# Performance work log

Hardware: AMD Instinct MI355X
Metric: run time of the kernel (lower is better)

The kernel has to match this reference:

```python
import jax, jax.numpy as jnp
import numpy as np

E, B, D, H, Z = 8, 16384, 512, 512, 64   # experts, batch, input_dim, hidden, latent
NHID = 2                                 # num_mlp_layers - 1 hidden-to-hidden layers


def setup_inputs() -> dict:
    key = jax.random.key(0)
    ks = jax.random.split(key, 12)

    def w(k, shape, fan_in):
        return (jax.random.normal(k, shape, jnp.float32) / np.sqrt(fan_in)).astype(jnp.float32)

    return {
        "x": jax.random.normal(ks[0], (B, D), jnp.float32),
        "eps": jax.random.normal(ks[1], (B, Z), jnp.float32),
        # stacked per-expert parameters (leading axis E)
        "enc_in_w": w(ks[2], (E, D, H), D), "enc_in_b": jnp.zeros((E, H), jnp.float32),
        "enc_hid_w": w(ks[3], (E, NHID, H, H), H), "enc_hid_b": jnp.zeros((E, NHID, H), jnp.float32),
        "mu_w": w(ks[4], (E, H, Z), H), "mu_b": jnp.zeros((E, Z), jnp.float32),
        "lv_w": w(ks[5], (E, H, Z), H), "lv_b": jnp.zeros((E, Z), jnp.float32),
        "dec_in_w": w(ks[6], (E, Z, H), Z), "dec_in_b": jnp.zeros((E, H), jnp.float32),
        "dec_hid_w": w(ks[7], (E, NHID, H, H), H), "dec_hid_b": jnp.zeros((E, NHID, H), jnp.float32),
        "dec_out_w": w(ks[8], (E, H, D), H), "dec_out_b": jnp.zeros((E, D), jnp.float32),
    }


def _moe_forward(x, eps, enc_in_w, enc_in_b, enc_hid_w, enc_hid_b,
                 mu_w, mu_b, lv_w, lv_b,
                 dec_in_w, dec_in_b, dec_hid_w, dec_hid_b, dec_out_w, dec_out_b):
    # ---- every expert tries the problem (dense, all experts over full batch) ----
    h = jax.nn.relu(jnp.einsum('bd,edh->ebh', x, enc_in_w) + enc_in_b[:, None, :])
    for i in range(NHID):
        h = jax.nn.relu(jnp.einsum('ebh,ehk->ebk', h, enc_hid_w[:, i]) + enc_hid_b[:, i, None, :])
    mu = jnp.einsum('ebh,ehz->ebz', h, mu_w) + mu_b[:, None, :]          # [E,B,Z]
    logvar = jnp.einsum('ebh,ehz->ebz', h, lv_w) + lv_b[:, None, :]       # [E,B,Z]
    z = mu + jnp.exp(0.5 * logvar) * eps[None, :, :]                      # reparameterize
    g = jax.nn.relu(jnp.einsum('ebz,ezh->ebh', z, dec_in_w) + dec_in_b[:, None, :])
    for i in range(NHID):
        g = jax.nn.relu(jnp.einsum('ebh,ehk->ebk', g, dec_hid_w[:, i]) + dec_hid_b[:, i, None, :])
    xhat = jnp.einsum('ebh,ehd->ebd', g, dec_out_w) + dec_out_b[:, None, :]  # [E,B,D]

    # ---- per-sample recon loss, pick best expert (torch.min over experts) ----
    recon = jnp.mean((xhat - x[None, :, :]) ** 2, axis=-1)                # [E,B]
    expert_idx = jnp.argmin(recon, axis=0)                                # [B]

    # ---- sparse_others: single fused gather instead of python loop ----
    bi = jnp.arange(x.shape[0])
    return mu[expert_idx, bi], logvar[expert_idx, bi], xhat[expert_idx, bi]


def reference(x, eps, enc_in_w, enc_in_b, enc_hid_w, enc_hid_b,
              mu_w, mu_b, lv_w, lv_b,
              dec_in_w, dec_in_b, dec_hid_w, dec_hid_b, dec_out_w, dec_out_b):
    return _moe_forward(x, eps, enc_in_w, enc_in_b, enc_hid_w, enc_hid_b,
                        mu_w, mu_b, lv_w, lv_b,
                        dec_in_w, dec_in_b, dec_hid_w, dec_hid_b, dec_out_w, dec_out_b)
```

## Files before the change

kernel.cpp:

```cpp
#include <hip/hip_runtime.h>
#include <cstdint>

#define Eexp 8
#define Bb   16384
#define Dd   512
#define Hh   512
#define Zz   64

typedef _Float16 f16x8 __attribute__((ext_vector_type(8)));
typedef float    f32x4 __attribute__((ext_vector_type(4)));

#define OFF_ENCIN  0
#define OFF_HID0   524288
#define OFF_HID1   1048576
#define OFF_HEADS  1572864
#define OFF_DECIN  1703936
#define OFF_DHID0  1769472
#define OFF_DHID1  2293760
#define OFF_DECOUT 2818048
#define PEREXP     3342336
#define WT_TOTAL   (8 * (size_t)PEREXP)

#define GLL16(g, l) __builtin_amdgcn_global_load_lds( \
    (const __attribute__((address_space(1))) void*)(g), \
    (__attribute__((address_space(3))) void*)(l), 16, 0, 0)

template<bool TR>
__global__ __launch_bounds__(256)
void fmsplit(const float* __restrict__ src, _Float16* __restrict__ dst,
             int KTOT, int inner, long sStride, long dStride)
{
    __shared__ float t[64][65];
    const int e  = blockIdx.z;
    const int o0 = blockIdx.x * 64;
    const int k0 = blockIdx.y * 64;
    const float* S = src + (size_t)e * sStride;
    _Float16*    D = dst + (size_t)e * dStride;
    const int tid = threadIdx.x;
    const int rr = tid >> 4, c4 = (tid & 15) * 4;
    #pragma unroll
    for (int p = 0; p < 4; ++p) {
        const int r = rr + p * 16;
        const float4 v = *reinterpret_cast<const float4*>(
            S + (size_t)(TR ? (k0 + r) : (o0 + r)) * inner + (TR ? o0 : k0) + c4);
        t[r][c4 + 0] = v.x; t[r][c4 + 1] = v.y;
        t[r][c4 + 2] = v.z; t[r][c4 + 3] = v.w;
    }
    __syncthreads();
    const int lane = tid & 63, wid = tid >> 6;
    const int KB = KTOT >> 5;
    #pragma unroll
    for (int p = 0; p < 2; ++p) {
        const int g  = wid * 2 + p;
        const int ot = g >> 1, kb = g & 1;
        const int rI = ot * 16 + (lane & 15);
        const int kI = kb * 32 + (lane >> 4) * 8;
        f16x8 hv, lv;
        #pragma unroll
        for (int j = 0; j < 8; ++j) {
            const float v = TR ? t[kI + j][rI] : t[rI][kI + j];
            const _Float16 h = (_Float16)v;
            hv[j] = h; lv[j] = (_Float16)(v - (float)h);
        }
        const size_t base = ((size_t)((o0 >> 4) + ot) * KB + (k0 >> 5) + kb) * 1024;
        *reinterpret_cast<f16x8*>(D + base + lane * 8)       = hv;
        *reinterpret_cast<f16x8*>(D + base + 512 + lane * 8) = lv;
    }
}

template<int KA>
__global__ __launch_bounds__(256, 2)
void gemm_mid(const _Float16* __restrict__ Afm, const _Float16* __restrict__ Wfm,
              const float* __restrict__ bias0, _Float16* __restrict__ Cfm)
{
    constexpr int KB  = KA / 32;
    constexpr int NT  = KB;
    constexpr int ACH = 16;
    constexpr int NCH = 32;
    constexpr int GPW = 8;
    __shared__ __align__(16) _Float16 lds[2 * NCH * 512];

    const int bid = blockIdx.x;
    const int bx = (bid & 7) * 16 + (bid >> 5);
    const int by = (bid >> 3) & 3;

    const int lane = threadIdx.x & 63, wid = threadIdx.x >> 6;
    const int wr = wid >> 1, wc = wid & 1;
    const int row0 = bx * 128;
    const int col0 = by * 128;

    const _Float16* src[GPW];
    #pragma unroll
    for (int p = 0; p < GPW; ++p) {
        const int q = wid * GPW + p;
        if (q < ACH)
            src[p] = Afm + (size_t)((row0 >> 4) + (q >> 1)) * KB * 1024
                         + (q & 1) * 512 + lane * 8;
        else {
            const int qq = q - ACH;
            src[p] = Wfm + (size_t)((col0 >> 4) + (qq >> 1)) * KB * 1024
                         + (qq & 1) * 512 + lane * 8;
        }
    }

    f32x4 acc[4][4];
    #pragma unroll
    for (int i = 0; i < 4; ++i)
        #pragma unroll
        for (int j = 0; j < 4; ++j) acc[i][j] = {0.f, 0.f, 0.f, 0.f};

#define STAGE(buf)                                                           \
    { _Pragma("unroll")                                                      \
      for (int p = 0; p < GPW; ++p) {                                        \
          GLL16(src[p], lds + (buf) * (NCH * 512) + (wid * GPW + p) * 512);  \
          src[p] += 1024;                                                    \
      } }

    STAGE(0)
    if (NT > 1) STAGE(1)

    for (int t = 0; t < NT; ++t) {
        if (t + 1 < NT) { asm volatile("s_waitcnt vmcnt(%0)" :: "i"(GPW) : "memory"); }
        else            { asm volatile("s_waitcnt vmcnt(0)" ::: "memory"); }
        __builtin_amdgcn_s_barrier();
        asm volatile("" ::: "memory");

        const _Float16* B0 = lds + (t & 1) * (NCH * 512);
        f16x8 ah[4], al[4], wh[4], wl[4];
        #pragma unroll
        for (int mf = 0; mf < 4; ++mf) {
            const int q = (wr * 4 + mf) * 2;
            ah[mf] = *reinterpret_cast<const f16x8*>(B0 + q * 512 + lane * 8);
            al[mf] = *reinterpret_cast<const f16x8*>(B0 + q * 512 + 512 + lane * 8);
        }
        #pragma unroll
        for (int nf = 0; nf < 4; ++nf) {
            const int q = ACH + (wc * 4 + nf) * 2;
            wh[nf] = *reinterpret_cast<const f16x8*>(B0 + q * 512 + lane * 8);
            wl[nf] = *reinterpret_cast<const f16x8*>(B0 + q * 512 + 512 + lane * 8);
        }
        __builtin_amdgcn_s_setprio(1);
        #pragma unroll
        for (int mf = 0; mf < 4; ++mf)
            #pragma unroll
            for (int nf = 0; nf < 4; ++nf) {
                acc[mf][nf] = __builtin_amdgcn_mfma_f32_16x16x32_f16(
                    ah[mf], wh[nf], acc[mf][nf], 0, 0, 0);
                acc[mf][nf] = __builtin_amdgcn_mfma_f32_16x16x32_f16(
                    ah[mf], wl[nf], acc[mf][nf], 0, 0, 0);
                acc[mf][nf] = __builtin_amdgcn_mfma_f32_16x16x32_f16(
                    al[mf], wh[nf], acc[mf][nf], 0, 0, 0);
            }
        __builtin_amdgcn_s_setprio(0);
        asm volatile("" ::: "memory");
        __builtin_amdgcn_s_barrier();
        asm volatile("" ::: "memory");
        if (t + 2 < NT) STAGE(t & 1)
    }
#undef STAGE

    uint32_t* sb = reinterpret_cast<uint32_t*>(&lds[0]);
    #pragma unroll
    for (int ph = 0; ph < 2; ++ph) {
        if (wc == ph) {
            #pragma unroll
            for (int nf = 0; nf < 4; ++nf) {
                const int c_l = nf * 16 + (lane & 15);
                const float bv = bias0[col0 + ph * 64 + c_l];
                #pragma unroll
                for (int mf = 0; mf < 4; ++mf)
                    #pragma unroll
                    for (int j = 0; j < 4; ++j) {
                        const int r_l = wr * 64 + mf * 16 + (lane >> 4) * 4 + j;
                        const float v = fmaxf(acc[mf][nf][j] + bv, 0.f);
                        const _Float16 h = (_Float16)v;
                        const _Float16 lo = (_Float16)(v - (float)h);
                        const uint32_t pk =
                            (uint32_t)__builtin_bit_cast(uint16_t, h) |
                            ((uint32_t)__builtin_bit_cast(uint16_t, lo) << 16);
                        sb[r_l * 64 + (((c_l >> 2) ^ (r_l & 15)) << 2) + (c_l & 3)] = pk;
                    }
            }
        }
        __syncthreads();
        {
            #pragma unroll
            for (int i = 0; i < 4; ++i) {
                const int q = wid * 4 + i;
                const int T_l = q >> 1, kb_l = q & 1;
                const int r_l = T_l * 16 + (lane & 15);
                const int cb  = kb_l * 32 + (lane >> 4) * 8;
                uint32_t u[8];
                #pragma unroll
                for (int jb = 0; jb < 2; ++jb) {
                    const int chunk = ((cb >> 2) + jb) ^ (r_l & 15);
                    const uint32_t* pp = &sb[r_l * 64 + chunk * 4];
                    u[jb*4+0] = pp[0]; u[jb*4+1] = pp[1];
                    u[jb*4+2] = pp[2]; u[jb*4+3] = pp[3];
                }
                f16x8 hv, lvv;
                #pragma unroll
                for (int j = 0; j < 8; ++j) {
                    hv[j]  = __builtin_bit_cast(_Float16, (uint16_t)(u[j] & 0xffff));
                    lvv[j] = __builtin_bit_cast(_Float16, (uint16_t)(u[j] >> 16));
                }
                const size_t base =
                    ((size_t)((row0 >> 4) + T_l) * 16 +
                     ((col0 + ph * 64) >> 5) + kb_l) * 1024;
                *reinterpret_cast<f16x8*>(Cfm + base + lane * 8)       = hv;
                *reinterpret_cast<f16x8*>(Cfm + base + 512 + lane * 8) = lvv;
            }
        }
        __syncthreads();
    }
}

__global__ __launch_bounds__(256, 2)
void heads_z(const _Float16* __restrict__ Afm, const _Float16* __restrict__ Wfm,
             const float* __restrict__ mu_b, const float* __restrict__ lv_b,
             const float* __restrict__ eps,
             float* __restrict__ mu_e, float* __restrict__ lv_e,
             _Float16* __restrict__ zfm)
{
    constexpr int KB = 16, NT = 16, ACH = 8, NCH = 24, GPW = 6;
    __shared__ __align__(16) _Float16 lds[2 * NCH * 512];

    const int bid = blockIdx.x;
    const int bx = (bid & 7) * 32 + (bid >> 3);
    const int lane = threadIdx.x & 63, wid = threadIdx.x >> 6;
    const int wr = wid >> 1, wc = wid & 1;
    const int row0 = bx * 64;

    const _Float16* src[GPW];
    #pragma unroll
    for (int p = 0; p < GPW; ++p) {
        const int q = wid * GPW + p;
        if (q < ACH)
            src[p] = Afm + (size_t)((row0 >> 4) + (q >> 1)) * KB * 1024
                         + (q & 1) * 512 + lane * 8;
        else {
            const int qq = q - ACH;
            src[p] = Wfm + (size_t)(qq >> 1) * KB * 1024 + (qq & 1) * 512 + lane * 8;
        }
    }

    f32x4 acc[2][4];
    #pragma unroll
    for (int i = 0; i < 2; ++i)
        #pragma unroll
        for (int j = 0; j < 4; ++j) acc[i][j] = {0.f, 0.f, 0.f, 0.f};

#define STAGE(buf)                                                           \
    { _Pragma("unroll")                                                      \
      for (int p = 0; p < GPW; ++p) {                                        \
          GLL16(src[p], lds + (buf) * (NCH * 512) + (wid * GPW + p) * 512);  \
          src[p] += 1024;                                                    \
      } }

    STAGE(0)
    STAGE(1)

    for (int t = 0; t < NT; ++t) {
        if (t + 1 < NT) { asm volatile("s_waitcnt vmcnt(%0)" :: "i"(GPW) : "memory"); }
        else            { asm volatile("s_waitcnt vmcnt(0)" ::: "memory"); }
        __builtin_amdgcn_s_barrier();
        asm volatile("" ::: "memory");

        const _Float16* B0 = lds + (t & 1) * (NCH * 512);
        f16x8 ah[2], al[2], wh[4], wl[4];
        #pragma unroll
        for (int mf = 0; mf < 2; ++mf) {
            const int q = (wr * 2 + mf) * 2;
            ah[mf] = *reinterpret_cast<const f16x8*>(B0 + q * 512 + lane * 8);
            al[mf] = *reinterpret_cast<const f16x8*>(B0 + q * 512 + 512 + lane * 8);
        }
        #pragma unroll
        for (int nf = 0; nf < 4; ++nf) {
            const int q = ACH + (wc * 4 + nf) * 2;
            wh[nf] = *reinterpret_cast<const f16x8*>(B0 + q * 512 + lane * 8);
            wl[nf] = *reinterpret_cast<const f16x8*>(B0 + q * 512 + 512 + lane * 8);
        }
        __builtin_amdgcn_s_setprio(1);
        #pragma unroll
        for (int mf = 0; mf < 2; ++mf)
            #pragma unroll
            for (int nf = 0; nf < 4; ++nf) {
                acc[mf][nf] = __builtin_amdgcn_mfma_f32_16x16x32_f16(
                    ah[mf], wh[nf], acc[mf][nf], 0, 0, 0);
                acc[mf][nf] = __builtin_amdgcn_mfma_f32_16x16x32_f16(
                    ah[mf], wl[nf], acc[mf][nf], 0, 0, 0);
                acc[mf][nf] = __builtin_amdgcn_mfma_f32_16x16x32_f16(
                    al[mf], wh[nf], acc[mf][nf], 0, 0, 0);
            }
        __builtin_amdgcn_s_setprio(0);
        asm volatile("" ::: "memory");
        __builtin_amdgcn_s_barrier();
        asm volatile("" ::: "memory");
        if (t + 2 < NT) STAGE(t & 1)
    }
#undef STAGE

    float* mulv = reinterpret_cast<float*>(&lds[0]);
    #pragma unroll
    for (int nf = 0; nf < 4; ++nf) {
        const int c_h = wc * 64 + nf * 16 + (lane & 15);
        const float bv = (c_h < 64) ? mu_b[c_h] : lv_b[c_h - 64];
        #pragma unroll
        for (int mf = 0; mf < 2; ++mf)
            #pragma unroll
            for (int j = 0; j < 4; ++j) {
                const int r_l = wr * 32 + mf * 16 + (lane >> 4) * 4 + j;
                mulv[r_l * 128 + c_h] = acc[mf][nf][j] + bv;
            }
    }
    __syncthreads();
    const int tid = threadIdx.x;
    #pragma unroll
    for (int k = 0; k < 16; ++k) {
        const int id  = tid + k * 256;
        const int r_l = id >> 6, c = id & 63;
        const float m = mulv[r_l * 128 + c];
        const float l = mulv[r_l * 128 + 64 + c];
        const size_t go = (size_t)(row0 + r_l) * 64 + c;
        const float ev = eps[go];
        const float z  = m + expf(0.5f * l) * ev;
        mu_e[go] = m; lv_e[go] = l;
        const _Float16 h  = (_Float16)z;
        const _Float16 lo = (_Float16)(z - (float)h);
        const size_t base = ((size_t)((row0 + r_l) >> 4) * 2 + (c >> 5)) * 1024
                            + ((r_l & 15) + ((c >> 3) & 3) * 16) * 8 + (c & 7);
        zfm[base]       = h;
        zfm[base + 512] = lo;
    }
}

__global__ __launch_bounds__(512, 1)
void dec_out_fused(const _Float16* __restrict__ Afm, const _Float16* __restrict__ Wfm,
                   const float* __restrict__ bias,
                   const float* __restrict__ Xin,
                   const float* __restrict__ mu_e, const float* __restrict__ lv_e,
                   float* __restrict__ best,
                   float* __restrict__ out_mu, float* __restrict__ out_lv,
                   float* __restrict__ out_xh, int isFirst)
{
    constexpr int KB = 16, NT = 16;
    __shared__ __align__(16) _Float16 lds[2 * 8 * 512];

    const int bid = blockIdx.x;
    const int bx = (bid & 7) * 32 + (bid >> 3);
    const int lane = threadIdx.x & 63, wid = threadIdx.x >> 6;
    const int row0 = bx * 64;
    const int colW = wid * 64;

    const _Float16* aSrc = Afm + (size_t)((row0 >> 4) + (wid >> 1)) * KB * 1024
                               + (wid & 1) * 512 + lane * 8;
    const _Float16* wSrc[8];
    #pragma unroll
    for (int i = 0; i < 8; ++i)
        wSrc[i] = Wfm + (size_t)(wid * 4 + (i >> 1)) * KB * 1024
                      + (i & 1) * 512 + lane * 8;

    f32x4 acc[4][4];
    #pragma unroll
    for (int i = 0; i < 4; ++i)
        #pragma unroll
        for (int j = 0; j < 4; ++j) acc[i][j] = {0.f, 0.f, 0.f, 0.f};

#define STAGE_A(buf)                                                         \
    { GLL16(aSrc, lds + (buf) * 4096 + wid * 512); aSrc += 1024; }

    STAGE_A(0)
    STAGE_A(1)

    for (int t = 0; t < NT; ++t) {
        f16x8 wh[4], wl[4];
        #pragma unroll
        for (int nf = 0; nf < 4; ++nf) {
            wh[nf] = *reinterpret_cast<const f16x8*>(wSrc[nf * 2]);
            wl[nf] = *reinterpret_cast<const f16x8*>(wSrc[nf * 2 + 1]);
            wSrc[nf * 2]     += 1024;
            wSrc[nf * 2 + 1] += 1024;
        }
        if (t + 1 < NT) { asm volatile("s_waitcnt vmcnt(9)" ::: "memory"); }
        else            { asm volatile("s_waitcnt vmcnt(8)" ::: "memory"); }
        __builtin_amdgcn_s_barrier();
        asm volatile("" ::: "memory");

        const _Float16* B0 = lds + (t & 1) * 4096;
        f16x8 ah[4], al[4];
        #pragma unroll
        for (int mf = 0; mf < 4; ++mf) {
            ah[mf] = *reinterpret_cast<const f16x8*>(B0 + mf * 1024 + lane * 8);
            al[mf] = *reinterpret_cast<const f16x8*>(B0 + mf * 1024 + 512 + lane * 8);
        }
        __builtin_amdgcn_s_setprio(1);
        #pragma unroll
        for (int mf = 0; mf < 4; ++mf)
            #pragma unroll
            for (int nf = 0; nf < 4; ++nf) {
                acc[mf][nf] = __builtin_amdgcn_mfma_f32_16x16x32_f16(
                    ah[mf], wh[nf], acc[mf][nf], 0, 0, 0);
                acc[mf][nf] = __builtin_amdgcn_mfma_f32_16x16x32_f16(
                    ah[mf], wl[nf], acc[mf][nf], 0, 0, 0);
                acc[mf][nf] = __builtin_amdgcn_mfma_f32_16x16x32_f16(
                    al[mf], wh[nf], acc[mf][nf], 0, 0, 0);
            }
        __builtin_amdgcn_s_setprio(0);
        asm volatile("" ::: "memory");
        __builtin_amdgcn_s_barrier();
        asm volatile("" ::: "memory");
        if (t + 2 < NT) STAGE_A(t & 1)
    }
#undef STAGE_A

    float* recP = reinterpret_cast<float*>(&lds[0]);
    int*   winf = reinterpret_cast<int*>(recP + 8 * 64);

    float rsum[4][4];
    #pragma unroll
    for (int mf = 0; mf < 4; ++mf)
        #pragma unroll
        for (int j = 0; j < 4; ++j) rsum[mf][j] = 0.f;
    float bv[4];
    #pragma unroll
    for (int nf = 0; nf < 4; ++nf) bv[nf] = bias[colW + nf * 16 + (lane & 15)];
    #pragma unroll
    for (int nf = 0; nf < 4; ++nf) {
        const int col = colW + nf * 16 + (lane & 15);
        #pragma unroll
        for (int mf = 0; mf < 4; ++mf)
            #pragma unroll
            for (int j = 0; j < 4; ++j) {
                const int r_l = mf * 16 + (lane >> 4) * 4 + j;
                const float v = acc[mf][nf][j] + bv[nf];
                const float d = v - Xin[(size_t)(row0 + r_l) * 512 + col];
                rsum[mf][j] += d * d;
            }
    }
    #pragma unroll
    for (int mf = 0; mf < 4; ++mf)
        #pragma unroll
        for (int j = 0; j < 4; ++j) {
            float s = rsum[mf][j];
            s += __shfl_xor(s, 1); s += __shfl_xor(s, 2);
            s += __shfl_xor(s, 4); s += __shfl_xor(s, 8);
            if ((lane & 15) == 0)
                recP[wid * 64 + mf * 16 + (lane >> 4) * 4 + j] = s;
        }
    __syncthreads();
    if (wid == 0) {
        float r = 0.f;
        #pragma unroll
        for (int w = 0; w < 8; ++w) r += recP[w * 64 + lane];
        const int grow = row0 + lane;
        const bool w = isFirst || (r < best[grow]);
        if (w) best[grow] = r;
        winf[lane] = w ? 1 : 0;
    }
    __syncthreads();
    #pragma unroll
    for (int mf = 0; mf < 4; ++mf)
        #pragma unroll
        for (int j = 0; j < 4; ++j) {
            const int r_l = mf * 16 + (lane >> 4) * 4 + j;
            if (winf[r_l]) {
                #pragma unroll
                for (int nf = 0; nf < 4; ++nf) {
                    const int col = colW + nf * 16 + (lane & 15);
                    out_xh[(size_t)(row0 + r_l) * 512 + col] = acc[mf][nf][j] + bv[nf];
                }
            }
        }
    #pragma unroll
    for (int k = 0; k < 8; ++k) {
        const int r = wid * 8 + k;
        if (winf[r]) {
            const size_t o = (size_t)(row0 + r) * 64 + lane;
            out_mu[o] = mu_e[o];
            out_lv[o] = lv_e[o];
        }
    }
}

extern "C" void kernel_launch(void* const* d_in, const int* in_sizes, int n_in,
                              void* d_out, int out_size, void* d_ws, size_t ws_size,
                              hipStream_t stream)
{
    const float* x         = (const float*)d_in[0];
    const float* eps       = (const float*)d_in[1];
    const float* enc_in_w  = (const float*)d_in[2];
    const float* enc_in_b  = (const float*)d_in[3];
    const float* enc_hid_w = (const float*)d_in[4];
    const float* enc_hid_b = (const float*)d_in[5];
    const float* mu_w      = (const float*)d_in[6];
    const float* mu_b      = (const float*)d_in[7];
    const float* lv_w      = (const float*)d_in[8];
    const float* lv_b      = (const float*)d_in[9];
    const float* dec_in_w  = (const float*)d_in[10];
    const float* dec_in_b  = (const float*)d_in[11];
    const float* dec_hid_w = (const float*)d_in[12];
    const float* dec_hid_b = (const float*)d_in[13];
    const float* dec_out_w = (const float*)d_in[14];
    const float* dec_out_b = (const float*)d_in[15];

    const size_t FM = (size_t)Bb * 512 * 2;
    const size_t BZ = (size_t)Bb * 64;

    _Float16* wt  = (_Float16*)d_ws;
    _Float16* xfm = wt + WT_TOTAL;
    _Float16* afm = xfm + FM;
    _Float16* bfm = afm + FM;
    _Float16* zfm = bfm + FM;
    float* fbase  = (float*)(zfm + (size_t)Bb * 64 * 2);
    float* mu_e   = fbase;
    float* lv_e   = mu_e + BZ;
    float* best   = lv_e + BZ;

    float* out_mu = (float*)d_out;
    float* out_lv = out_mu + (size_t)Bb * Zz;
    float* out_xh = out_lv + (size_t)Bb * Zz;

    const dim3 blk(256);

    fmsplit<true ><<<dim3(8, 8, 8), blk, 0, stream>>>(enc_in_w,           wt + OFF_ENCIN,  512, 512, 262144, PEREXP);
    fmsplit<true ><<<dim3(8, 8, 8), blk, 0, stream>>>(enc_hid_w,          wt + OFF_HID0,   512, 512, 524288, PEREXP);
    fmsplit<true ><<<dim3(8, 8, 8), blk, 0, stream>>>(enc_hid_w + 262144, wt + OFF_HID1,   512, 512, 524288, PEREXP);
    fmsplit<true ><<<dim3(1, 8, 8), blk, 0, stream>>>(mu_w,               wt + OFF_HEADS,  512,  64,  32768, PEREXP);
    fmsplit<true ><<<dim3(1, 8, 8), blk, 0, stream>>>(lv_w,        wt + OFF_HEADS + 65536, 512,  64,  32768, PEREXP);
    fmsplit<true ><<<dim3(8, 1, 8), blk, 0, stream>>>(dec_in_w,           wt + OFF_DECIN,   64, 512,  32768, PEREXP);
    fmsplit<true ><<<dim3(8, 8, 8), blk, 0, stream>>>(dec_hid_w,          wt + OFF_DHID0,  512, 512, 524288, PEREXP);
    fmsplit<true ><<<dim3(8, 8, 8), blk, 0, stream>>>(dec_hid_w + 262144, wt + OFF_DHID1,  512, 512, 524288, PEREXP);
    fmsplit<true ><<<dim3(8, 8, 8), blk, 0, stream>>>(dec_out_w,          wt + OFF_DECOUT, 512, 512, 262144, PEREXP);
    fmsplit<false><<<dim3(256, 8, 1), blk, 0, stream>>>(x,                xfm,             512, 512, 0, 0);

    const dim3 g512(512), g256(256), blk512(512);

    for (int e = 0; e < Eexp; ++e) {
        const _Float16* we = wt + (size_t)e * PEREXP;
        gemm_mid<512><<<g512, blk, 0, stream>>>(
            xfm, we + OFF_ENCIN, enc_in_b + (size_t)e * Hh, afm);
        gemm_mid<512><<<g512, blk, 0, stream>>>(
            afm, we + OFF_HID0, enc_hid_b + ((size_t)e * 2 + 0) * Hh, bfm);
        gemm_mid<512><<<g512, blk, 0, stream>>>(
            bfm, we + OFF_HID1, enc_hid_b + ((size_t)e * 2 + 1) * Hh, afm);
        heads_z<<<g256, blk, 0, stream>>>(
            afm, we + OFF_HEADS, mu_b + (size_t)e * Zz, lv_b + (size_t)e * Zz,
            eps, mu_e, lv_e, zfm);
        gemm_mid< 64><<<g512, blk, 0, stream>>>(
            zfm, we + OFF_DECIN, dec_in_b + (size_t)e * Hh, bfm);
        gemm_mid<512><<<g512, blk, 0, stream>>>(
            bfm, we + OFF_DHID0, dec_hid_b + ((size_t)e * 2 + 0) * Hh, afm);
        gemm_mid<512><<<g512, blk, 0, stream>>>(
            afm, we + OFF_DHID1, dec_hid_b + ((size_t)e * 2 + 1) * Hh, bfm);
        dec_out_fused<<<g256, blk512, 0, stream>>>(
            bfm, we + OFF_DECOUT, dec_out_b + (size_t)e * Dd,
            x, mu_e, lv_e, best, out_mu, out_lv, out_xh, e == 0 ? 1 : 0);
    }
}
```

Before: 1.683 ms.

## Batch two experts per launch via grid y-dimension for mid GEMMs and heads

```diff
diff --git a/kernel.cpp b/kernel.cpp
--- a/kernel.cpp
+++ b/kernel.cpp
@@ -20,6 +20,9 @@
 #define OFF_DECOUT 2818048
 #define PEREXP     3342336
 #define WT_TOTAL   (8 * (size_t)PEREXP)
+#define FMELEMS    ((size_t)Bb * 512 * 2)
+#define ZFME       ((size_t)Bb * 64 * 2)
+#define BZE        ((size_t)Bb * 64)
 
 #define GLL16(g, l) __builtin_amdgcn_global_load_lds( \
     (const __attribute__((address_space(1))) void*)(g), \
@@ -70,8 +73,10 @@
 
 template<int KA>
 __global__ __launch_bounds__(256, 2)
-void gemm_mid(const _Float16* __restrict__ Afm, const _Float16* __restrict__ Wfm,
-              const float* __restrict__ bias0, _Float16* __restrict__ Cfm)
+void gemm_mid(const _Float16* __restrict__ Afm, size_t aStr,
+              const _Float16* __restrict__ Wfm,
+              const float* __restrict__ bias0, size_t bStr,
+              _Float16* __restrict__ Cfm)
 {
     constexpr int KB  = KA / 32;
     constexpr int NT  = KB;
@@ -80,6 +85,12 @@
     constexpr int GPW = 8;
     __shared__ __align__(16) _Float16 lds[2 * NCH * 512];
 
+    const int z = blockIdx.y;
+    const _Float16* A = Afm + (size_t)z * aStr;
+    const _Float16* W = Wfm + (size_t)z * PEREXP;
+    const float*    B = bias0 + (size_t)z * bStr;
+    _Float16*       C = Cfm + (size_t)z * FMELEMS;
+
     const int bid = blockIdx.x;
     const int bx = (bid & 7) * 16 + (bid >> 5);
     const int by = (bid >> 3) & 3;
@@ -94,12 +105,12 @@
     for (int p = 0; p < GPW; ++p) {
         const int q = wid * GPW + p;
         if (q < ACH)
-            src[p] = Afm + (size_t)((row0 >> 4) + (q >> 1)) * KB * 1024
-                         + (q & 1) * 512 + lane * 8;
+            src[p] = A + (size_t)((row0 >> 4) + (q >> 1)) * KB * 1024
+                       + (q & 1) * 512 + lane * 8;
         else {
             const int qq = q - ACH;
-            src[p] = Wfm + (size_t)((col0 >> 4) + (qq >> 1)) * KB * 1024
-                         + (qq & 1) * 512 + lane * 8;
+            src[p] = W + (size_t)((col0 >> 4) + (qq >> 1)) * KB * 1024
+                       + (qq & 1) * 512 + lane * 8;
         }
     }
 
@@ -166,7 +177,7 @@
             #pragma unroll
             for (int nf = 0; nf < 4; ++nf) {
                 const int c_l = nf * 16 + (lane & 15);
-                const float bv = bias0[col0 + ph * 64 + c_l];
+                const float bv = B[col0 + ph * 64 + c_l];
                 #pragma unroll
                 for (int mf = 0; mf < 4; ++mf)
                     #pragma unroll
@@ -207,8 +218,8 @@
                 const size_t base =
                     ((size_t)((row0 >> 4) + T_l) * 16 +
                      ((col0 + ph * 64) >> 5) + kb_l) * 1024;
-                *reinterpret_cast<f16x8*>(Cfm + base + lane * 8)       = hv;
-                *reinterpret_cast<f16x8*>(Cfm + base + 512 + lane * 8) = lvv;
+                *reinterpret_cast<f16x8*>(C + base + lane * 8)       = hv;
+                *reinterpret_cast<f16x8*>(C + base + 512 + lane * 8) = lvv;
             }
         }
         __syncthreads();
@@ -217,13 +228,22 @@
 
 __global__ __launch_bounds__(256, 2)
 void heads_z(const _Float16* __restrict__ Afm, const _Float16* __restrict__ Wfm,
-             const float* __restrict__ mu_b, const float* __restrict__ lv_b,
+             const float* __restrict__ mu_bp, const float* __restrict__ lv_bp,
              const float* __restrict__ eps,
-             float* __restrict__ mu_e, float* __restrict__ lv_e,
-             _Float16* __restrict__ zfm)
+             float* __restrict__ mu_ep, float* __restrict__ lv_ep,
+             _Float16* __restrict__ zfmp)
 {
     constexpr int KB = 16, NT = 16, ACH = 8, NCH = 24, GPW = 6;
     __shared__ __align__(16) _Float16 lds[2 * NCH * 512];
+
+    const int z = blockIdx.y;
+    const _Float16* A = Afm + (size_t)z * FMELEMS;
+    const _Float16* W = Wfm + (size_t)z * PEREXP;
+    const float* mu_b = mu_bp + (size_t)z * Zz;
+    const float* lv_b = lv_bp + (size_t)z * Zz;
+    float* mu_e = mu_ep + (size_t)z * BZE;
+    float* lv_e = lv_ep + (size_t)z * BZE;
+    _Float16* zfm = zfmp + (size_t)z * ZFME;
 
     const int bid = blockIdx.x;
     const int bx = (bid & 7) * 32 + (bid >> 3);
@@ -236,11 +256,11 @@
     for (int p = 0; p < GPW; ++p) {
         const int q = wid * GPW + p;
         if (q < ACH)
-            src[p] = Afm + (size_t)((row0 >> 4) + (q >> 1)) * KB * 1024
-                         + (q & 1) * 512 + lane * 8;
+            src[p] = A + (size_t)((row0 >> 4) + (q >> 1)) * KB * 1024
+                       + (q & 1) * 512 + lane * 8;
         else {
             const int qq = q - ACH;
-            src[p] = Wfm + (size_t)(qq >> 1) * KB * 1024 + (qq & 1) * 512 + lane * 8;
+            src[p] = W + (size_t)(qq >> 1) * KB * 1024 + (qq & 1) * 512 + lane * 8;
         }
     }
 
@@ -323,10 +343,10 @@
         const float l = mulv[r_l * 128 + 64 + c];
         const size_t go = (size_t)(row0 + r_l) * 64 + c;
         const float ev = eps[go];
-        const float z  = m + expf(0.5f * l) * ev;
+        const float zv = m + expf(0.5f * l) * ev;
         mu_e[go] = m; lv_e[go] = l;
-        const _Float16 h  = (_Float16)z;
-        const _Float16 lo = (_Float16)(z - (float)h);
+        const _Float16 h  = (_Float16)zv;
+        const _Float16 lo = (_Float16)(zv - (float)h);
         const size_t base = ((size_t)((row0 + r_l) >> 4) * 2 + (c >> 5)) * 1024
                             + ((r_l & 15) + ((c >> 3) & 3) * 16) * 8 + (c & 7);
         zfm[base]       = h;
@@ -503,18 +523,15 @@
     const float* dec_out_w = (const float*)d_in[14];
     const float* dec_out_b = (const float*)d_in[15];
 
-    const size_t FM = (size_t)Bb * 512 * 2;
-    const size_t BZ = (size_t)Bb * 64;
-
     _Float16* wt  = (_Float16*)d_ws;
     _Float16* xfm = wt + WT_TOTAL;
-    _Float16* afm = xfm + FM;
-    _Float16* bfm = afm + FM;
-    _Float16* zfm = bfm + FM;
-    float* fbase  = (float*)(zfm + (size_t)Bb * 64 * 2);
+    _Float16* afm = xfm + FMELEMS;
+    _Float16* bfm = afm + 2 * FMELEMS;
+    _Float16* zfm = bfm + 2 * FMELEMS;
+    float* fbase  = (float*)(zfm + 2 * ZFME);
     float* mu_e   = fbase;
-    float* lv_e   = mu_e + BZ;
-    float* best   = lv_e + BZ;
+    float* lv_e   = mu_e + 2 * BZE;
+    float* best   = lv_e + 2 * BZE;
 
     float* out_mu = (float*)d_out;
     float* out_lv = out_mu + (size_t)Bb * Zz;
@@ -533,27 +550,38 @@
     fmsplit<true ><<<dim3(8, 8, 8), blk, 0, stream>>>(dec_out_w,          wt + OFF_DECOUT, 512, 512, 262144, PEREXP);
     fmsplit<false><<<dim3(256, 8, 1), blk, 0, stream>>>(x,                xfm,             512, 512, 0, 0);
 
-    const dim3 g512(512), g256(256), blk512(512);
-
-    for (int e = 0; e < Eexp; ++e) {
-        const _Float16* we = wt + (size_t)e * PEREXP;
-        gemm_mid<512><<<g512, blk, 0, stream>>>(
-            xfm, we + OFF_ENCIN, enc_in_b + (size_t)e * Hh, afm);
-        gemm_mid<512><<<g512, blk, 0, stream>>>(
-            afm, we + OFF_HID0, enc_hid_b + ((size_t)e * 2 + 0) * Hh, bfm);
-        gemm_mid<512><<<g512, blk, 0, stream>>>(
-            bfm, we + OFF_HID1, enc_hid_b + ((size_t)e * 2 + 1) * Hh, afm);
-        heads_z<<<g256, blk, 0, stream>>>(
-            afm, we + OFF_HEADS, mu_b + (size_t)e * Zz, lv_b + (size_t)e * Zz,
+    const dim3 g512x2(512, 2), g256x2(256, 2), g256(256), blk512(512);
+
+    for (int ep = 0; ep < 4; ++ep) {
+        const int e0 = ep * 2;
+        const _Float16* we = wt + (size_t)e0 * PEREXP;
+        gemm_mid<512><<<g512x2, blk, 0, stream>>>(
+            xfm, 0, we + OFF_ENCIN, enc_in_b + (size_t)e0 * Hh, Hh, afm);
+        gemm_mid<512><<<g512x2, blk, 0, stream>>>(
+            afm, FMELEMS, we + OFF_HID0,
+            enc_hid_b + (size_t)e0 * 2 * Hh, 2 * Hh, bfm);
+        gemm_mid<512><<<g512x2, blk, 0, stream>>>(
+            bfm, FMELEMS, we + OFF_HID1,
+            enc_hid_b + ((size_t)e0 * 2 + 1) * Hh, 2 * Hh, afm);
+        heads_z<<<g256x2, blk, 0, stream>>>(
+            afm, we + OFF_HEADS, mu_b + (size_t)e0 * Zz, lv_b + (size_t)e0 * Zz,
             eps, mu_e, lv_e, zfm);
-        gemm_mid< 64><<<g512, blk, 0, stream>>>(
-            zfm, we + OFF_DECIN, dec_in_b + (size_t)e * Hh, bfm);
-        gemm_mid<512><<<g512, blk, 0, stream>>>(
-            bfm, we + OFF_DHID0, dec_hid_b + ((size_t)e * 2 + 0) * Hh, afm);
-        gemm_mid<512><<<g512, blk, 0, stream>>>(
-            afm, we + OFF_DHID1, dec_hid_b + ((size_t)e * 2 + 1) * Hh, bfm);
-        dec_out_fused<<<g256, blk512, 0, stream>>>(
-            bfm, we + OFF_DECOUT, dec_out_b + (size_t)e * Dd,
-            x, mu_e, lv_e, best, out_mu, out_lv, out_xh, e == 0 ? 1 : 0);
+        gemm_mid< 64><<<g512x2, blk, 0, stream>>>(
+            zfm, ZFME, we + OFF_DECIN, dec_in_b + (size_t)e0 * Hh, Hh, bfm);
+        gemm_mid<512><<<g512x2, blk, 0, stream>>>(
+            bfm, FMELEMS, we + OFF_DHID0,
+            dec_hid_b + (size_t)e0 * 2 * Hh, 2 * Hh, afm);
+        gemm_mid<512><<<g512x2, blk, 0, stream>>>(
+            afm, FMELEMS, we + OFF_DHID1,
+            dec_hid_b + ((size_t)e0 * 2 + 1) * Hh, 2 * Hh, bfm);
+        for (int q = 0; q < 2; ++q) {
+            const int e = e0 + q;
+            dec_out_fused<<<g256, blk512, 0, stream>>>(
+                bfm + (size_t)q * FMELEMS,
+                wt + (size_t)e * PEREXP + OFF_DECOUT,
+                dec_out_b + (size_t)e * Dd,
+                x, mu_e + (size_t)q * BZE, lv_e + (size_t)q * BZE,
+                best, out_mu, out_lv, out_xh, e == 0 ? 1 : 0);
+        }
     }
 }
```

After: 1.733 ms. +2.9%, slower.
